# Performance work log

Measured on AMD Instinct MI355X. Metric: run time of the kernel, lower is better.

The kernel has to match this reference:

```python
import math
import jax, jax.numpy as jnp
import numpy as np

HEADS = 8

def relative_shift(score):
    # score: [B, H, S, 2S-1] -> [B, H, S, S] via Music Transformer skew trick
    B, H, S, R = score.shape
    score = jnp.pad(score, ((0, 0), (0, 0), (0, 0), (1, 0)))          # [B,H,S,2S]
    score = score.reshape(B, H, -1)[:, :, S:].reshape(B, H, S, -1)    # [B,H,S,2S-1]
    return score[..., :S]


def setup_inputs() -> dict:
    B, S, D = 4, 1024, 512
    dh = D // HEADS
    rng = jax.random.key(0)
    ks = jax.random.split(rng, 14)
    w = 0.02  # init scale
    return {
        "query":   jax.random.normal(ks[0], (B, S, D), jnp.float32),
        "key":     jax.random.normal(ks[1], (B, S, D), jnp.float32),
        "value":   jax.random.normal(ks[2], (B, S, D), jnp.float32),
        "pos_emb": jax.random.normal(ks[3], (2 * S - 1, dh), jnp.float32),
        "Wq": jax.random.normal(ks[4], (D, D), jnp.float32) * w,
        "bq": jnp.zeros((D,), jnp.float32),
        "Wk": jax.random.normal(ks[5], (D, D), jnp.float32) * w,
        "bk": jnp.zeros((D,), jnp.float32),
        "Wv": jax.random.normal(ks[6], (D, D), jnp.float32) * w,
        "bv": jnp.zeros((D,), jnp.float32),
        "Wo": jax.random.normal(ks[7], (D, D), jnp.float32) * w,
        "bo": jnp.zeros((D,), jnp.float32),
        "Wp": jax.random.normal(ks[8], (dh, dh), jnp.float32) * w,
        "bp": jnp.zeros((dh,), jnp.float32),
    }


def reference(query, key, value, pos_emb, Wq, bq, Wk, bk, Wv, bv, Wo, bo, Wp, bp):
    B, S, D = query.shape
    H = HEADS
    dh = D // H
    q = (query @ Wq.T + bq).reshape(B, S, H, dh).transpose(0, 2, 1, 3)  # [B,H,S,dh]
    k = (key   @ Wk.T + bk).reshape(B, S, H, dh).transpose(0, 2, 1, 3)  # [B,H,S,dh]
    v = (value @ Wv.T + bv).reshape(B, S, H, dh).transpose(0, 2, 1, 3)  # [B,H,S,dh]
    rel = pos_emb @ Wp.T + bp                                           # [2S-1, dh]

    pos_score = jnp.einsum('bhsd,rd->bhsr', q, rel)                     # [B,H,S,2S-1]
    pos_score = relative_shift(pos_score)                               # [B,H,S,S]
    content_score = jnp.einsum('bhsd,bhtd->bhst', q, k)                 # [B,H,S,S]
    score = (content_score + pos_score) / math.sqrt(D)                  # scale by sqrt(d_model)
    attn = jax.nn.softmax(score, axis=-1)
    out = jnp.einsum('bhst,bhtd->bshd', attn, v).reshape(B, S, D)
    return (out @ Wo.T + bo, attn, content_score, pos_score)
```

## Files before the change

### kernel.cpp

```cpp
#include <hip/hip_runtime.h>

typedef __attribute__((ext_vector_type(8))) short short8;
typedef __attribute__((ext_vector_type(4))) float f32x4;
typedef __attribute__((ext_vector_type(2))) float f32x2;
typedef unsigned short u16;
typedef unsigned int u32;

#define MFMA16(a, b, c) __builtin_amdgcn_mfma_f32_16x16x32_bf16((a), (b), (c), 0, 0, 0)
#define SCALE 0.044194173824159216f

#define SCX(r, c) ((c) ^ (((r) & 7) << 2))
#define PAX(r, c) ((c) ^ (((r) & 7) << 3))

__device__ __forceinline__ u16 f2bf(float f) {
    u32 u = __float_as_uint(f);
    u = (u + 0x7fffu + ((u >> 16) & 1u)) >> 16;
    return (u16)u;
}

__global__ __launch_bounds__(256) void cvt_kernel(const float* __restrict__ src,
                                                  u16* __restrict__ dst, int n4) {
    int i = blockIdx.x * 256 + threadIdx.x;
    if (i >= n4) return;
    float4 v = ((const float4*)src)[i];
    unsigned long long p = (unsigned long long)f2bf(v.x)
                         | ((unsigned long long)f2bf(v.y) << 16)
                         | ((unsigned long long)f2bf(v.z) << 32)
                         | ((unsigned long long)f2bf(v.w) << 48);
    ((unsigned long long*)dst)[i] = p;
}

__global__ __launch_bounds__(256) void rel_kernel(const float* __restrict__ pos_emb,
                                                  const float* __restrict__ Wp,
                                                  const float* __restrict__ bp,
                                                  u16* __restrict__ rel) {
    int idx = blockIdx.x * 256 + threadIdx.x;
    if (idx >= 2047 * 64) return;
    int r = idx >> 6, c = idx & 63;
    const float* pe = pos_emb + r * 64;
    const float* w  = Wp + c * 64;
    float acc = bp[c];
#pragma unroll
    for (int k = 0; k < 64; k++) acc += pe[k] * w[k];
    rel[r * 64 + c] = f2bf(acc);
}

template <int MODE>
__global__ __launch_bounds__(256) void gemm_kernel(const u16* __restrict__ A,
                                                   const u16* __restrict__ B,
                                                   const float* __restrict__ bias,
                                                   void* __restrict__ Cout,
                                                   int M, int N, int K) {
    int tid = threadIdx.x;
    int w = tid >> 6, lane = tid & 63;
    int wi = w >> 1, wj = w & 1;
    int qd = lane >> 4, ln = lane & 15;
    int m_base = blockIdx.x * 64 + wi * 32;
    int n_base = blockIdx.y * 64 + wj * 32;
    f32x4 acc[2][2] = {};
    const u16* a0p = A + (long)(m_base + ln) * K + qd * 8;
    const u16* a1p = a0p + 16 * K;
    const u16* b0p = B + (long)(n_base + ln) * K + qd * 8;
    const u16* b1p = b0p + 16 * K;
    for (int kc = 0; kc < K; kc += 32) {
        short8 a0 = *(const short8*)(a0p + kc);
        short8 a1 = *(const short8*)(a1p + kc);
        short8 b0 = *(const short8*)(b0p + kc);
        short8 b1 = *(const short8*)(b1p + kc);
        acc[0][0] = MFMA16(a0, b0, acc[0][0]);
        acc[0][1] = MFMA16(a0, b1, acc[0][1]);
        acc[1][0] = MFMA16(a1, b0, acc[1][0]);
        acc[1][1] = MFMA16(a1, b1, acc[1][1]);
    }
#pragma unroll
    for (int i = 0; i < 2; i++)
#pragma unroll
        for (int j = 0; j < 2; j++)
#pragma unroll
            for (int r = 0; r < 4; r++) {
                int m = m_base + i * 16 + qd * 4 + r;
                int n = n_base + j * 16 + ln;
                float v = acc[i][j][r];
                if (MODE == 0) {
                    v += bias[n];
                    int b = m >> 10, s = m & 1023, h = n >> 6, d = n & 63;
                    ((u16*)Cout)[(((long)(b * 8 + h) << 10) + s) * 64 + d] = f2bf(v);
                } else if (MODE == 1) {
                    v += bias[m];
                    int b = n >> 10, t = n & 1023, h = m >> 6, d = m & 63;
                    ((u16*)Cout)[(((long)(b * 8 + h) * 64 + d) << 10) + t] = f2bf(v);
                } else {
                    v += bias[n];
                    ((float*)Cout)[(long)m * N + n] = v;
                }
            }
}

__global__ __launch_bounds__(256) void score_kernel(const u16* __restrict__ qws,
                                                    const u16* __restrict__ kws,
                                                    const u16* __restrict__ vtws,
                                                    const u16* __restrict__ relws,
                                                    float* __restrict__ out_attn,
                                                    float* __restrict__ out_cont,
                                                    float* __restrict__ out_pos,
                                                    u16* __restrict__ ctx) {
    __shared__ __align__(16) float sc[16][1024];
    u16* pa = (u16*)sc;
    int st = blockIdx.x, h = blockIdx.y, b = blockIdx.z;
    int s0 = st * 16;
    int tid = threadIdx.x;
    int w = tid >> 6, lane = tid & 63, qd = lane >> 4, ln = lane & 15;
    int bh = b * 8 + h;

    const u16* qbase  = qws + ((long)bh << 10) * 64;
    const u16* kbase  = kws + ((long)bh << 10) * 64;
    const u16* vtbase = vtws + ((long)bh << 6) * 1024;
    float* attn_base = out_attn + ((long)bh << 20) + (long)s0 * 1024;
    float* cont_base = out_cont + ((long)bh << 20) + (long)s0 * 1024;
    float* pos_base  = out_pos  + ((long)bh << 20) + (long)s0 * 1024;

    short8 qa0 = *(const short8*)(qbase + (s0 + ln) * 64 + qd * 8);
    short8 qa1 = *(const short8*)(qbase + (s0 + ln) * 64 + 32 + qd * 8);

    for (int tt = 0; tt < 16; tt++) {
        int t0 = w * 256 + tt * 16;
        short8 kb0 = *(const short8*)(kbase + (t0 + ln) * 64 + qd * 8);
        short8 kb1 = *(const short8*)(kbase + (t0 + ln) * 64 + 32 + qd * 8);
        f32x4 acc = {};
        acc = MFMA16(qa0, kb0, acc);
        acc = MFMA16(qa1, kb1, acc);
#pragma unroll
        for (int r = 0; r < 4; r++) {
            int sl = qd * 4 + r;
            int t = t0 + ln;
            cont_base[sl * 1024 + t] = acc[r];
            sc[sl][SCX(sl, t)] = acc[r] * SCALE;
        }
    }
    __syncthreads();

    int rbase = 1008 - s0;
    for (int rt = w; rt < 65; rt += 4) {
        int r0 = rbase + rt * 16;
        short8 rb0 = *(const short8*)(relws + (r0 + ln) * 64 + qd * 8);
        short8 rb1 = *(const short8*)(relws + (r0 + ln) * 64 + 32 + qd * 8);
        f32x4 acc = {};
        acc = MFMA16(qa0, rb0, acc);
        acc = MFMA16(qa1, rb1, acc);
#pragma unroll
        for (int r = 0; r < 4; r++) {
            int sl = qd * 4 + r;
            int t = rt * 16 + ln + sl - 15;
            if (t >= 0 && t < 1024) {
                pos_base[sl * 1024 + t] = acc[r];
                sc[sl][SCX(sl, t)] += acc[r] * SCALE;
            }
        }
    }
    __syncthreads();

    {
        int row = tid >> 4;
        int g = tid & 15;
        float ev[64];
        float mx = -1e30f;
#pragma unroll
        for (int i = 0; i < 32; i++) {
            int c = 2 * g + 32 * i;
            f32x2 v = *(const f32x2*)&sc[row][SCX(row, c)];
            ev[2 * i] = v[0];
            ev[2 * i + 1] = v[1];
            mx = fmaxf(mx, fmaxf(v[0], v[1]));
        }
        for (int off = 1; off < 16; off <<= 1) mx = fmaxf(mx, __shfl_xor(mx, off, 64));
        float sum = 0.f;
#pragma unroll
        for (int i = 0; i < 64; i++) {
            float e = __expf(ev[i] - mx);
            ev[i] = e;
            sum += e;
        }
        for (int off = 1; off < 16; off <<= 1) sum += __shfl_xor(sum, off, 64);
        float inv = 1.0f / sum;
        __syncthreads();
#pragma unroll
        for (int i = 0; i < 32; i++) {
            int c = 2 * g + 32 * i;
            float a0 = ev[2 * i] * inv;
            float a1 = ev[2 * i + 1] * inv;
            f32x2 av = {a0, a1};
            *(f32x2*)&attn_base[row * 1024 + c] = av;
            u32 pk;
            asm("v_cvt_pk_bf16_f32 %0, %1, %2" : "=v"(pk) : "v"(a0), "v"(a1));
            *(u32*)&pa[row * 1024 + PAX(row, c)] = pk;
        }
    }
    __syncthreads();

    {
        const u16* vrow = vtbase + (w * 16 + ln) * 1024 + qd * 8;
        f32x4 oacc = {};
        for (int kt = 0; kt < 32; kt++) {
            int c = kt * 32 + qd * 8;
            short8 a = *(const short8*)&pa[ln * 1024 + PAX(ln, c)];
            short8 bf = *(const short8*)(vrow + kt * 32);
            oacc = MFMA16(a, bf, oacc);
        }
#pragma unroll
        for (int r = 0; r < 4; r++) {
            int sl = qd * 4 + r;
            int d = w * 16 + ln;
            ctx[((long)(b * 1024 + s0 + sl)) * 512 + h * 64 + d] = f2bf(oacc[r]);
        }
    }
}

extern "C" void kernel_launch(void* const* d_in, const int* in_sizes, int n_in,
                              void* d_out, int out_size, void* d_ws, size_t ws_size,
                              hipStream_t stream) {
    (void)in_sizes; (void)n_in; (void)out_size; (void)ws_size;
    const float* query   = (const float*)d_in[0];
    const float* key     = (const float*)d_in[1];
    const float* value   = (const float*)d_in[2];
    const float* pos_emb = (const float*)d_in[3];
    const float* Wq = (const float*)d_in[4];
    const float* bq = (const float*)d_in[5];
    const float* Wk = (const float*)d_in[6];
    const float* bk = (const float*)d_in[7];
    const float* Wv = (const float*)d_in[8];
    const float* bv = (const float*)d_in[9];
    const float* Wo = (const float*)d_in[10];
    const float* bo = (const float*)d_in[11];
    const float* Wp = (const float*)d_in[12];
    const float* bp = (const float*)d_in[13];

    u16* qin  = (u16*)d_ws;
    u16* kin  = qin + 4096 * 512;
    u16* vin  = kin + 4096 * 512;
    u16* wqb  = vin + 4096 * 512;
    u16* wkb  = wqb + 512 * 512;
    u16* wvb  = wkb + 512 * 512;
    u16* wob  = wvb + 512 * 512;
    u16* relb = wob + 512 * 512;
    u16* qws  = relb + 2048 * 64;
    u16* kws  = qws + 4 * 8 * 1024 * 64;
    u16* vtws = kws + 4 * 8 * 1024 * 64;
    u16* ctx  = qin;

    float* out  = (float*)d_out;
    float* attn = out + 2097152;
    float* cont = attn + 33554432;
    float* pos  = cont + 33554432;

    cvt_kernel<<<2048, 256, 0, stream>>>(query, qin, 524288);
    cvt_kernel<<<2048, 256, 0, stream>>>(key, kin, 524288);
    cvt_kernel<<<2048, 256, 0, stream>>>(value, vin, 524288);
    cvt_kernel<<<256, 256, 0, stream>>>(Wq, wqb, 65536);
    cvt_kernel<<<256, 256, 0, stream>>>(Wk, wkb, 65536);
    cvt_kernel<<<256, 256, 0, stream>>>(Wv, wvb, 65536);
    cvt_kernel<<<256, 256, 0, stream>>>(Wo, wob, 65536);
    rel_kernel<<<512, 256, 0, stream>>>(pos_emb, Wp, bp, relb);

    gemm_kernel<0><<<dim3(64, 8), 256, 0, stream>>>(qin, wqb, bq, qws, 4096, 512, 512);
    gemm_kernel<0><<<dim3(64, 8), 256, 0, stream>>>(kin, wkb, bk, kws, 4096, 512, 512);
    gemm_kernel<1><<<dim3(8, 64), 256, 0, stream>>>(wvb, vin, bv, vtws, 512, 4096, 512);

    score_kernel<<<dim3(64, 8, 4), 256, 0, stream>>>(qws, kws, vtws, relb, attn, cont, pos, ctx);

    gemm_kernel<2><<<dim3(64, 8), 256, 0, stream>>>(ctx, wob, bo, out, 4096, 512, 512);
}
```

Baseline: 225.2 us.

## Chunk score kernel over keys, drop max-subtraction softmax, overlap PV with scoring

The score kernel now processes keys in four 256-wide chunks with a smaller float scratch and a separate bf16 probability buffer. It computes exp without subtracting the row max and accumulates the row sum incrementally. The PV MFMA for the previous chunk is interleaved with scoring of the next, and normalisation is deferred to the end. This cuts LDS use (which may allow more resident blocks) and removes a full softmax pass. The cost is that skipping the max subtraction risks overflow for large scores, and the attention output is now rebuilt from bf16-rounded exponentials, which loses precision.

```diff
diff --git a/kernel.cpp b/kernel.cpp
--- a/kernel.cpp
+++ b/kernel.cpp
@@ -104,12 +104,14 @@
                                                     float* __restrict__ out_cont,
                                                     float* __restrict__ out_pos,
                                                     u16* __restrict__ ctx) {
-    __shared__ __align__(16) float sc[16][1024];
-    u16* pa = (u16*)sc;
+    __shared__ __align__(16) float sc[16][256];
+    __shared__ __align__(16) u16 pa[16][1024];
+    __shared__ float sinv[16];
     int st = blockIdx.x, h = blockIdx.y, b = blockIdx.z;
     int s0 = st * 16;
     int tid = threadIdx.x;
     int w = tid >> 6, lane = tid & 63, qd = lane >> 4, ln = lane & 15;
+    int row = tid >> 4, g = tid & 15;
     int bh = b * 8 + h;
 
     const u16* qbase  = qws + ((long)bh << 10) * 64;
@@ -122,96 +124,99 @@
     short8 qa0 = *(const short8*)(qbase + (s0 + ln) * 64 + qd * 8);
     short8 qa1 = *(const short8*)(qbase + (s0 + ln) * 64 + 32 + qd * 8);
 
-    for (int tt = 0; tt < 16; tt++) {
-        int t0 = w * 256 + tt * 16;
-        short8 kb0 = *(const short8*)(kbase + (t0 + ln) * 64 + qd * 8);
-        short8 kb1 = *(const short8*)(kbase + (t0 + ln) * 64 + 32 + qd * 8);
-        f32x4 acc = {};
-        acc = MFMA16(qa0, kb0, acc);
-        acc = MFMA16(qa1, kb1, acc);
-#pragma unroll
-        for (int r = 0; r < 4; r++) {
-            int sl = qd * 4 + r;
-            int t = t0 + ln;
-            cont_base[sl * 1024 + t] = acc[r];
-            sc[sl][SCX(sl, t)] = acc[r] * SCALE;
-        }
-    }
+    int rbase = 1008 - s0;
+    float lsum = 0.f;
+    f32x4 oa0 = {}, oa1 = {};
+    const u16* vbase2 = vtbase + (w * 16 + ln) * 1024 + qd * 8;
+
+    auto p4_partial = [&](int p0) {
+#pragma unroll
+        for (int kt = 0; kt < 8; kt++) {
+            int c = p0 + kt * 32;
+            short8 a = *(const short8*)&pa[ln][PAX(ln, c + qd * 8)];
+            short8 bf = *(const short8*)(vbase2 + c);
+            if (kt & 1) oa1 = MFMA16(a, bf, oa1);
+            else        oa0 = MFMA16(a, bf, oa0);
+        }
+    };
+
+    for (int ck = 0; ck < 4; ck++) {
+        int c0 = ck * 256;
+        if (ck > 0) p4_partial(c0 - 256);
+        for (int tt = 0; tt < 4; tt++) {
+            int t0 = c0 + w * 64 + tt * 16;
+            const u16* kp = kbase + (t0 + ln) * 64 + qd * 8;
+            short8 kb0 = *(const short8*)(kp);
+            short8 kb1 = *(const short8*)(kp + 32);
+            f32x4 acc = {};
+            acc = MFMA16(qa0, kb0, acc);
+            acc = MFMA16(qa1, kb1, acc);
+#pragma unroll
+            for (int r = 0; r < 4; r++) {
+                int sl = qd * 4 + r;
+                int t = t0 + ln;
+                cont_base[sl * 1024 + t] = acc[r];
+                sc[sl][SCX(sl, t - c0)] = acc[r] * SCALE;
+            }
+        }
+        __syncthreads();
+        for (int rt = 16 * ck + w; rt <= 16 * ck + 16; rt += 4) {
+            int r0 = rbase + rt * 16;
+            const u16* rp = relws + (r0 + ln) * 64 + qd * 8;
+            short8 rb0 = *(const short8*)(rp);
+            short8 rb1 = *(const short8*)(rp + 32);
+            f32x4 acc = {};
+            acc = MFMA16(qa0, rb0, acc);
+            acc = MFMA16(qa1, rb1, acc);
+#pragma unroll
+            for (int r = 0; r < 4; r++) {
+                int sl = qd * 4 + r;
+                int t = rt * 16 + ln + sl - 15;
+                if (t >= c0 && t < c0 + 256) {
+                    pos_base[sl * 1024 + t] = acc[r];
+                    sc[sl][SCX(sl, t - c0)] += acc[r] * SCALE;
+                }
+            }
+        }
+        __syncthreads();
+#pragma unroll
+        for (int i = 0; i < 8; i++) {
+            int cl = 2 * g + 32 * i;
+            f32x2 vv = *(const f32x2*)&sc[row][SCX(row, cl)];
+            float e0 = __expf(vv[0]);
+            float e1 = __expf(vv[1]);
+            lsum += e0 + e1;
+            u32 pk;
+            asm("v_cvt_pk_bf16_f32 %0, %1, %2" : "=v"(pk) : "v"(e0), "v"(e1));
+            *(u32*)&pa[row][PAX(row, c0 + cl)] = pk;
+        }
+        __syncthreads();
+    }
+
+    p4_partial(768);
+    for (int off = 1; off < 16; off <<= 1) lsum += __shfl_xor(lsum, off, 64);
+    if (g == 0) sinv[row] = 1.0f / lsum;
     __syncthreads();
 
-    int rbase = 1008 - s0;
-    for (int rt = w; rt < 65; rt += 4) {
-        int r0 = rbase + rt * 16;
-        short8 rb0 = *(const short8*)(relws + (r0 + ln) * 64 + qd * 8);
-        short8 rb1 = *(const short8*)(relws + (r0 + ln) * 64 + 32 + qd * 8);
-        f32x4 acc = {};
-        acc = MFMA16(qa0, rb0, acc);
-        acc = MFMA16(qa1, rb1, acc);
-#pragma unroll
-        for (int r = 0; r < 4; r++) {
-            int sl = qd * 4 + r;
-            int t = rt * 16 + ln + sl - 15;
-            if (t >= 0 && t < 1024) {
-                pos_base[sl * 1024 + t] = acc[r];
-                sc[sl][SCX(sl, t)] += acc[r] * SCALE;
-            }
-        }
-    }
-    __syncthreads();
-
     {
-        int row = tid >> 4;
-        int g = tid & 15;
-        float ev[64];
-        float mx = -1e30f;
+        float inv = sinv[row];
 #pragma unroll
         for (int i = 0; i < 32; i++) {
             int c = 2 * g + 32 * i;
-            f32x2 v = *(const f32x2*)&sc[row][SCX(row, c)];
-            ev[2 * i] = v[0];
-            ev[2 * i + 1] = v[1];
-            mx = fmaxf(mx, fmaxf(v[0], v[1]));
-        }
-        for (int off = 1; off < 16; off <<= 1) mx = fmaxf(mx, __shfl_xor(mx, off, 64));
-        float sum = 0.f;
-#pragma unroll
-        for (int i = 0; i < 64; i++) {
-            float e = __expf(ev[i] - mx);
-            ev[i] = e;
-            sum += e;
-        }
-        for (int off = 1; off < 16; off <<= 1) sum += __shfl_xor(sum, off, 64);
-        float inv = 1.0f / sum;
-        __syncthreads();
-#pragma unroll
-        for (int i = 0; i < 32; i++) {
-            int c = 2 * g + 32 * i;
-            float a0 = ev[2 * i] * inv;
-            float a1 = ev[2 * i + 1] * inv;
-            f32x2 av = {a0, a1};
+            u32 pk = *(const u32*)&pa[row][PAX(row, c)];
+            float lo = __uint_as_float(pk << 16);
+            float hi = __uint_as_float(pk & 0xffff0000u);
+            f32x2 av = {lo * inv, hi * inv};
             *(f32x2*)&attn_base[row * 1024 + c] = av;
-            u32 pk;
-            asm("v_cvt_pk_bf16_f32 %0, %1, %2" : "=v"(pk) : "v"(a0), "v"(a1));
-            *(u32*)&pa[row * 1024 + PAX(row, c)] = pk;
-        }
-    }
-    __syncthreads();
-
-    {
-        const u16* vrow = vtbase + (w * 16 + ln) * 1024 + qd * 8;
-        f32x4 oacc = {};
-        for (int kt = 0; kt < 32; kt++) {
-            int c = kt * 32 + qd * 8;
-            short8 a = *(const short8*)&pa[ln * 1024 + PAX(ln, c)];
-            short8 bf = *(const short8*)(vrow + kt * 32);
-            oacc = MFMA16(a, bf, oacc);
-        }
-#pragma unroll
-        for (int r = 0; r < 4; r++) {
-            int sl = qd * 4 + r;
-            int d = w * 16 + ln;
-            ctx[((long)(b * 1024 + s0 + sl)) * 512 + h * 64 + d] = f2bf(oacc[r]);
-        }
+        }
+    }
+
+#pragma unroll
+    for (int r = 0; r < 4; r++) {
+        int sl = qd * 4 + r;
+        float o = (oa0[r] + oa1[r]) * sinv[sl];
+        int d = w * 16 + ln;
+        ctx[((long)(b * 1024 + s0 + sl)) * 512 + h * 64 + d] = f2bf(o);
     }
 }
 
```

New measurement: 237.3 us. 1.05x slower.
